# Kernel optimization log

Hardware: AMD Instinct MI355X
Metric: run time of the kernel (lower is better)

## Reference

```python
import jax, jax.numpy as jnp
import numpy as np

DVEC = 128
B, S = 4, 1024


def setup_inputs() -> dict:
    key = jax.random.key(0)
    k1, k2 = jax.random.split(key)
    func_and_arg = jax.random.normal(k1, (B, S, 2 * DVEC), dtype=jnp.float32)
    cooccurrences = jax.random.normal(k2, (DVEC, DVEC, DVEC), dtype=jnp.float32)
    return {"func_and_arg": func_and_arg, "cooccurrences": cooccurrences}


def reference(func_and_arg, cooccurrences):
    # out[b,s,z] = sum_{i,j} func[b,s,i] * cooc[i,j,z] * arg[b,s,j]
    d = cooccurrences.shape[0]
    func = func_and_arg[..., :d]   # [B,S,D]
    arg = func_and_arg[..., d:]    # [B,S,D]
    # contract func over i first -> [B,S,D(j),Z], then arg over j -> [B,S,Z]
    tmp = jnp.einsum('bsi,ijz->bsjz', func, cooccurrences)
    return jnp.einsum('bsjz,bsj->bsz', tmp, arg)
```

## Files before the change

### kernel.cpp

```cpp
#include <hip/hip_runtime.h>
#include <hip/hip_bf16.h>


typedef __attribute__((ext_vector_type(8))) short bf16x8;
typedef __attribute__((ext_vector_type(4))) float f32x4;

__device__ __forceinline__ unsigned pkbf16(float x, float y) {
    __hip_bfloat162 h = __float22bfloat162_rn(make_float2(x, y));
    unsigned u; __builtin_memcpy(&u, &h, sizeof(u));
    return u;
}

__global__ __launch_bounds__(256) void cooc_transpose(
    const float* __restrict__ Cc, ushort* __restrict__ CT)
{
    __shared__ float tile[32][132];
    const int i  = blockIdx.x >> 2;
    const int j0 = (blockIdx.x & 3) * 32;
    const int t  = threadIdx.x;
    {
        const int jj = t >> 3;
        const int zb = (t & 7) * 16;
        const float* src = Cc + (size_t)i * 16384 + (size_t)(j0 + jj) * 128 + zb;
        #pragma unroll
        for (int k = 0; k < 4; ++k)
            *(float4*)&tile[jj][zb + k * 4] = *(const float4*)(src + k * 4);
    }
    __syncthreads();
    {
        const int z = t >> 1;
        const int h = t & 1;
        unsigned o[8];
        #pragma unroll
        for (int p = 0; p < 8; ++p)
            o[p] = pkbf16(tile[h * 16 + 2 * p][z], tile[h * 16 + 2 * p + 1][z]);
        const int c0 = (j0 >> 3) + h * 2;
        ushort* dst = CT + (size_t)i * 16384 + (size_t)(z >> 4) * 2048
                         + (size_t)c0 * 128 + (z & 15) * 8;
        *(uint4*)dst         = make_uint4(o[0], o[1], o[2], o[3]);
        *(uint4*)(dst + 128) = make_uint4(o[4], o[5], o[6], o[7]);
    }
}

__global__ __launch_bounds__(256) void cooc_apack(
    const float* __restrict__ fa, ushort* __restrict__ APK)
{
    const int g = blockIdx.x;
    const int t = threadIdx.x;
    const int ks = t >> 6, lk = (t >> 4) & 3, lm = t & 15;
    const float* src = fa + (size_t)(g * 16 + lm) * 256 + 128 + ks * 32 + lk * 8;
    float4 q0 = *(const float4*)src;
    float4 q1 = *(const float4*)(src + 4);
    unsigned o0 = pkbf16(q0.x, q0.y), o1 = pkbf16(q0.z, q0.w);
    unsigned o2 = pkbf16(q1.x, q1.y), o3 = pkbf16(q1.z, q1.w);
    *(uint4*)(APK + (size_t)g * 2048 + t * 8) = make_uint4(o0, o1, o2, o3);
}

template<int USE_WS>
__global__ __launch_bounds__(256, 2) void cooc_main(
    const float* __restrict__ fa, const ushort* __restrict__ CT,
    const ushort* __restrict__ APK, float* __restrict__ dst)
{
    __shared__ float f_lds[16][128];

    const int bid = blockIdx.x;
    const int kp = bid & 7, zp = (bid >> 3) & 1, mtile = bid >> 4;
    const int t0 = mtile * 128, i0 = kp * 16, z0 = zp * 64;
    const int tid = threadIdx.x, lane = tid & 63, wv = tid >> 6;
    const int lm = lane & 15, lk = lane >> 4;

    {
        const int row = tid & 127;
        const int sh = (tid >> 7) * 8;
        const float* fp = fa + (size_t)(t0 + row) * 256 + i0 + sh;
        float4 v0 = *(const float4*)fp;
        float4 v1 = *(const float4*)(fp + 4);
        f_lds[sh + 0][row] = v0.x; f_lds[sh + 1][row] = v0.y;
        f_lds[sh + 2][row] = v0.z; f_lds[sh + 3][row] = v0.w;
        f_lds[sh + 4][row] = v1.x; f_lds[sh + 5][row] = v1.y;
        f_lds[sh + 6][row] = v1.z; f_lds[sh + 7][row] = v1.w;
    }

    bf16x8 a_pk[8][4];
    {
        const ushort* ap = APK + (size_t)(t0 >> 4) * 2048 + lane * 8;
        #pragma unroll
        for (int m = 0; m < 8; ++m)
            #pragma unroll
            for (int ks = 0; ks < 4; ++ks)
                a_pk[m][ks] = *(const bf16x8*)(ap + (size_t)m * 2048 + ks * 512);
    }
    __syncthreads();

    const ushort* bsrc = CT + (size_t)i0 * 16384
                            + (size_t)(zp * 4 + wv) * 2048 + lane * 8;

    bf16x8 B[2][4];
    #pragma unroll
    for (int ks = 0; ks < 4; ++ks)
        B[0][ks] = *(const bf16x8*)(bsrc + ks * 512);

    float acc[8][4];
    #pragma unroll
    for (int m = 0; m < 8; ++m)
        #pragma unroll
        for (int r = 0; r < 4; ++r) acc[m][r] = 0.f;

    #pragma unroll 2
    for (int s = 0; s < 16; ++s) {
        const int cur = s & 1;
        if (s < 15) {
            const ushort* p = bsrc + (size_t)(s + 1) * 16384;
            #pragma unroll
            for (int ks = 0; ks < 4; ++ks)
                B[cur ^ 1][ks] = *(const bf16x8*)(p + ks * 512);
        }
        #pragma unroll
        for (int h = 0; h < 2; ++h) {
            float4 f4[4];
            #pragma unroll
            for (int mm = 0; mm < 4; ++mm)
                f4[mm] = *(const float4*)&f_lds[s][(h * 4 + mm) * 16 + lk * 4];

            f32x4 g[4];
            #pragma unroll
            for (int mm = 0; mm < 4; ++mm) g[mm] = (f32x4){0.f, 0.f, 0.f, 0.f};

            #pragma unroll
            for (int ks = 0; ks < 4; ++ks)
                #pragma unroll
                for (int mm = 0; mm < 4; ++mm)
                    g[mm] = __builtin_amdgcn_mfma_f32_16x16x32_bf16(
                        a_pk[h * 4 + mm][ks], B[cur][ks], g[mm], 0, 0, 0);

            #pragma unroll
            for (int mm = 0; mm < 4; ++mm) {
                acc[h * 4 + mm][0] += f4[mm].x * g[mm][0];
                acc[h * 4 + mm][1] += f4[mm].y * g[mm][1];
                acc[h * 4 + mm][2] += f4[mm].z * g[mm][2];
                acc[h * 4 + mm][3] += f4[mm].w * g[mm][3];
            }
        }
    }

    const int col = z0 + wv * 16 + lm;
    #pragma unroll
    for (int m = 0; m < 8; ++m)
        #pragma unroll
        for (int r = 0; r < 4; ++r) {
            const int row = t0 + m * 16 + lk * 4 + r;
            if (USE_WS)
                dst[(size_t)kp * 524288 + (size_t)row * 128 + col] = acc[m][r];
            else
                atomicAdd(&dst[(size_t)row * 128 + col], acc[m][r]);
        }
}

__global__ __launch_bounds__(256) void cooc_reduce(const float* __restrict__ ws,
                                                   float* __restrict__ out) {
    const size_t idx = ((size_t)blockIdx.x * 256 + threadIdx.x) * 4;
    float4 a = *(const float4*)(ws + idx);
    #pragma unroll
    for (int k = 1; k < 8; ++k) {
        float4 b = *(const float4*)(ws + (size_t)k * 524288 + idx);
        a.x += b.x; a.y += b.y; a.z += b.z; a.w += b.w;
    }
    *(float4*)(out + idx) = a;
}

extern "C" void kernel_launch(void* const* d_in, const int* in_sizes, int n_in,
                              void* d_out, int out_size, void* d_ws, size_t ws_size,
                              hipStream_t stream) {
    const float* fa = (const float*)d_in[0];
    const float* Cc = (const float*)d_in[1];
    float* out = (float*)d_out;

    const size_t PART = (size_t)8 * 524288;
    const size_t CTOF = PART * sizeof(float);
    const size_t CTSZ = (size_t)128 * 128 * 128 * 2;
    const size_t APOF = CTOF + CTSZ;
    const size_t APSZ = (size_t)4096 * 128 * 2;
    const size_t NEED_FULL = APOF + APSZ;
    const size_t NEED_CT   = CTSZ + APSZ;

    if (ws_size >= NEED_FULL) {
        ushort* CT  = (ushort*)((char*)d_ws + CTOF);
        ushort* APK = (ushort*)((char*)d_ws + APOF);
        cooc_transpose<<<512, 256, 0, stream>>>(Cc, CT);
        cooc_apack<<<256, 256, 0, stream>>>(fa, APK);
        cooc_main<1><<<512, 256, 0, stream>>>(fa, CT, APK, (float*)d_ws);
        cooc_reduce<<<512, 256, 0, stream>>>((const float*)d_ws, out);
    } else if (ws_size >= NEED_CT) {
        ushort* CT  = (ushort*)d_ws;
        ushort* APK = (ushort*)((char*)d_ws + CTSZ);
        cooc_transpose<<<512, 256, 0, stream>>>(Cc, CT);
        cooc_apack<<<256, 256, 0, stream>>>(fa, APK);
        (void)hipMemsetAsync(out, 0, (size_t)out_size * sizeof(float), stream);
        cooc_main<0><<<512, 256, 0, stream>>>(fa, CT, APK, out);
    } else {
        (void)hipMemsetAsync(out, 0, (size_t)out_size * sizeof(float), stream);
        cooc_main<0><<<512, 256, 0, stream>>>(fa, (const ushort*)d_ws,
                                              (const ushort*)d_ws, out);
    }
}
```

Before: 89.03 us.

## Split waves over M and Z halves, double grid, deepen B prefetch

Each block now covers 32 output columns instead of 64, and its four waves are arranged as 2 M-groups by 2 Z-groups, so each wave holds half as many A fragments and accumulators. The grid doubles to 1024 blocks, and the launch bound asks for 3 blocks per CU to raise occupancy. B fragments are now prefetched two slices ahead. The cost is that each A fragment load and the f_lds staging are repeated across more blocks, and global reloads of APK and fa increase.

```diff
diff --git a/kernel.cpp b/kernel.cpp
--- a/kernel.cpp
+++ b/kernel.cpp
@@ -57,16 +57,17 @@
 }
 
 template<int USE_WS>
-__global__ __launch_bounds__(256, 2) void cooc_main(
+__global__ __launch_bounds__(256, 3) void cooc_main(
     const float* __restrict__ fa, const ushort* __restrict__ CT,
     const ushort* __restrict__ APK, float* __restrict__ dst)
 {
     __shared__ float f_lds[16][128];
 
     const int bid = blockIdx.x;
-    const int kp = bid & 7, zp = (bid >> 3) & 1, mtile = bid >> 4;
-    const int t0 = mtile * 128, i0 = kp * 16, z0 = zp * 64;
+    const int kp = bid & 7, zp = (bid >> 3) & 3, mtile = bid >> 5;
+    const int t0 = mtile * 128, i0 = kp * 16;
     const int tid = threadIdx.x, lane = tid & 63, wv = tid >> 6;
+    const int mg = wv >> 1, zg = wv & 1;
     const int lm = lane & 15, lk = lane >> 4;
 
     {
@@ -81,11 +82,11 @@
         f_lds[sh + 6][row] = v1.z; f_lds[sh + 7][row] = v1.w;
     }
 
-    bf16x8 a_pk[8][4];
-    {
-        const ushort* ap = APK + (size_t)(t0 >> 4) * 2048 + lane * 8;
-        #pragma unroll
-        for (int m = 0; m < 8; ++m)
+    bf16x8 a_pk[4][4];
+    {
+        const ushort* ap = APK + (size_t)((t0 >> 4) + mg * 4) * 2048 + lane * 8;
+        #pragma unroll
+        for (int m = 0; m < 4; ++m)
             #pragma unroll
             for (int ks = 0; ks < 4; ++ks)
                 a_pk[m][ks] = *(const bf16x8*)(ap + (size_t)m * 2048 + ks * 512);
@@ -93,62 +94,61 @@
     __syncthreads();
 
     const ushort* bsrc = CT + (size_t)i0 * 16384
-                            + (size_t)(zp * 4 + wv) * 2048 + lane * 8;
+                            + (size_t)(zp * 2 + zg) * 2048 + lane * 8;
 
     bf16x8 B[2][4];
     #pragma unroll
-    for (int ks = 0; ks < 4; ++ks)
+    for (int ks = 0; ks < 4; ++ks) {
         B[0][ks] = *(const bf16x8*)(bsrc + ks * 512);
-
-    float acc[8][4];
-    #pragma unroll
-    for (int m = 0; m < 8; ++m)
+        B[1][ks] = *(const bf16x8*)(bsrc + 16384 + ks * 512);
+    }
+
+    float acc[4][4];
+    #pragma unroll
+    for (int m = 0; m < 4; ++m)
         #pragma unroll
         for (int r = 0; r < 4; ++r) acc[m][r] = 0.f;
 
     #pragma unroll 2
     for (int s = 0; s < 16; ++s) {
         const int cur = s & 1;
-        if (s < 15) {
-            const ushort* p = bsrc + (size_t)(s + 1) * 16384;
+
+        f32x4 g[4];
+        #pragma unroll
+        for (int m = 0; m < 4; ++m) g[m] = (f32x4){0.f, 0.f, 0.f, 0.f};
+        #pragma unroll
+        for (int ks = 0; ks < 4; ++ks)
+            #pragma unroll
+            for (int m = 0; m < 4; ++m)
+                g[m] = __builtin_amdgcn_mfma_f32_16x16x32_bf16(
+                    a_pk[m][ks], B[cur][ks], g[m], 0, 0, 0);
+
+        if (s < 14) {
+            const ushort* p = bsrc + (size_t)(s + 2) * 16384;
             #pragma unroll
             for (int ks = 0; ks < 4; ++ks)
-                B[cur ^ 1][ks] = *(const bf16x8*)(p + ks * 512);
+                B[cur][ks] = *(const bf16x8*)(p + ks * 512);
         }
-        #pragma unroll
-        for (int h = 0; h < 2; ++h) {
-            float4 f4[4];
-            #pragma unroll
-            for (int mm = 0; mm < 4; ++mm)
-                f4[mm] = *(const float4*)&f_lds[s][(h * 4 + mm) * 16 + lk * 4];
-
-            f32x4 g[4];
-            #pragma unroll
-            for (int mm = 0; mm < 4; ++mm) g[mm] = (f32x4){0.f, 0.f, 0.f, 0.f};
-
-            #pragma unroll
-            for (int ks = 0; ks < 4; ++ks)
-                #pragma unroll
-                for (int mm = 0; mm < 4; ++mm)
-                    g[mm] = __builtin_amdgcn_mfma_f32_16x16x32_bf16(
-                        a_pk[h * 4 + mm][ks], B[cur][ks], g[mm], 0, 0, 0);
-
-            #pragma unroll
-            for (int mm = 0; mm < 4; ++mm) {
-                acc[h * 4 + mm][0] += f4[mm].x * g[mm][0];
-                acc[h * 4 + mm][1] += f4[mm].y * g[mm][1];
-                acc[h * 4 + mm][2] += f4[mm].z * g[mm][2];
-                acc[h * 4 + mm][3] += f4[mm].w * g[mm][3];
-            }
+
+        float4 f4[4];
+        #pragma unroll
+        for (int m = 0; m < 4; ++m)
+            f4[m] = *(const float4*)&f_lds[s][mg * 64 + m * 16 + lk * 4];
+        #pragma unroll
+        for (int m = 0; m < 4; ++m) {
+            acc[m][0] += f4[m].x * g[m][0];
+            acc[m][1] += f4[m].y * g[m][1];
+            acc[m][2] += f4[m].z * g[m][2];
+            acc[m][3] += f4[m].w * g[m][3];
         }
     }
 
-    const int col = z0 + wv * 16 + lm;
-    #pragma unroll
-    for (int m = 0; m < 8; ++m)
+    const int col = zp * 32 + zg * 16 + lm;
+    #pragma unroll
+    for (int m = 0; m < 4; ++m)
         #pragma unroll
         for (int r = 0; r < 4; ++r) {
-            const int row = t0 + m * 16 + lk * 4 + r;
+            const int row = t0 + mg * 64 + m * 16 + lk * 4 + r;
             if (USE_WS)
                 dst[(size_t)kp * 524288 + (size_t)row * 128 + col] = acc[m][r];
             else
@@ -188,7 +188,7 @@
         ushort* APK = (ushort*)((char*)d_ws + APOF);
         cooc_transpose<<<512, 256, 0, stream>>>(Cc, CT);
         cooc_apack<<<256, 256, 0, stream>>>(fa, APK);
-        cooc_main<1><<<512, 256, 0, stream>>>(fa, CT, APK, (float*)d_ws);
+        cooc_main<1><<<1024, 256, 0, stream>>>(fa, CT, APK, (float*)d_ws);
         cooc_reduce<<<512, 256, 0, stream>>>((const float*)d_ws, out);
     } else if (ws_size >= NEED_CT) {
         ushort* CT  = (ushort*)d_ws;
@@ -196,10 +196,10 @@
         cooc_transpose<<<512, 256, 0, stream>>>(Cc, CT);
         cooc_apack<<<256, 256, 0, stream>>>(fa, APK);
         (void)hipMemsetAsync(out, 0, (size_t)out_size * sizeof(float), stream);
-        cooc_main<0><<<512, 256, 0, stream>>>(fa, CT, APK, out);
+        cooc_main<0><<<1024, 256, 0, stream>>>(fa, CT, APK, out);
     } else {
         (void)hipMemsetAsync(out, 0, (size_t)out_size * sizeof(float), stream);
-        cooc_main<0><<<512, 256, 0, stream>>>(fa, (const ushort*)d_ws,
-                                              (const ushort*)d_ws, out);
-    }
-}
+        cooc_main<0><<<1024, 256, 0, stream>>>(fa, (const ushort*)d_ws,
+                                               (const ushort*)d_ws, out);
+    }
+}
```

After: 86.22 us. -3.2%, faster.
